# Kernel optimization log

Hardware: AMD Instinct MI355X
Metric: run time of the kernel (lower is better)

The kernel has to match this reference:

```python
import jax, jax.numpy as jnp
import numpy as np

FORGET_BIAS = 1.0

def _lstm_scan(x_seq, W, b, c0, h0):
    """x_seq: [T, B, D]; W: [D+H, 4H] (gate order i,j,f,o as in BasicLSTMCell)."""
    def step(carry, x_t):
        c, h = carry
        gates = jnp.dot(jnp.concatenate([x_t, h], axis=-1), W) + b  # [B, 4H]
        i, j, f, o = jnp.split(gates, 4, axis=-1)
        c_new = c * jax.nn.sigmoid(f + FORGET_BIAS) + jax.nn.sigmoid(i) * jnp.tanh(j)
        h_new = jnp.tanh(c_new) * jax.nn.sigmoid(o)
        return (c_new, h_new), h_new
    (c_T, h_T), hs = jax.lax.scan(step, (c0, h0), x_seq)
    return hs, (c_T, h_T)


def setup_inputs() -> dict:
    key = jax.random.key(0)
    ks = jax.random.split(key, 10)
    B, T_enc, D_in = 128, 64, 2048
    T_dec, D_w, H, V = 32, 300, 512, 32000
    s = lambda fan_in: 1.0 / np.sqrt(fan_in)
    return {
        "frames": jax.random.normal(ks[0], (B, T_enc, D_in), dtype=jnp.float32),
        "caption_ids": jax.random.randint(ks[1], (B, T_dec), 0, V, dtype=jnp.int32),
        "emb_table": jax.random.normal(ks[2], (V, D_w), dtype=jnp.float32) * 0.1,
        "W_enc": jax.random.normal(ks[3], (D_in + H, 4 * H), dtype=jnp.float32) * s(D_in + H),
        "b_enc": jnp.zeros((4 * H,), dtype=jnp.float32),
        "W_dec": jax.random.normal(ks[4], (D_w + H, 4 * H), dtype=jnp.float32) * s(D_w + H),
        "b_dec": jnp.zeros((4 * H,), dtype=jnp.float32),
        "W_out": jax.random.normal(ks[5], (H, D_w), dtype=jnp.float32) * s(H),
        "b_out": jnp.zeros((D_w,), dtype=jnp.float32),
    }


def reference(frames, caption_ids, emb_table, W_enc, b_enc, W_dec, b_dec, W_out, b_out):
    B, _, _ = frames.shape
    H = W_out.shape[0]
    c0 = jnp.zeros((B, H), dtype=frames.dtype)
    h0 = jnp.zeros((B, H), dtype=frames.dtype)

    # Encoder: dynamic_rnn over frames (dropout keep_prob=1 -> identity)
    _, enc_state = _lstm_scan(jnp.swapaxes(frames, 0, 1), W_enc, b_enc, c0, h0)

    # Decoder: teacher-forced over caption embeddings, starting from encoder state
    cap_emb = emb_table[caption_ids]                       # [B, T_dec, D_w]
    dec_hs, _ = _lstm_scan(jnp.swapaxes(cap_emb, 0, 1), W_dec, b_dec, *enc_state)  # [T_dec, B, H]

    # hidden_to_word dense per timestep
    word_vecs = jnp.einsum('tbh,hw->tbw', dec_hs, W_out) + b_out  # [T_dec, B, D_w]
    return jnp.swapaxes(word_vecs, 0, 1)                   # [B, T_dec, D_w]
```

## Files before the change

kernel.cpp:

```cpp
#include <hip/hip_runtime.h>
#include <stdint.h>

typedef unsigned short u16;
typedef __attribute__((ext_vector_type(4))) float f32x4;
typedef __attribute__((ext_vector_type(8))) short short8;
typedef __attribute__((ext_vector_type(4))) unsigned short u16x4;
typedef __attribute__((ext_vector_type(4))) int int4v;

__device__ __forceinline__ u16 f2b(float f) {
  uint32_t u = __float_as_uint(f);
  uint32_t r = (u + 0x7fffu + ((u >> 16) & 1u)) >> 16;
  return (u16)r;
}
__device__ __forceinline__ float b2f(u16 b) {
  return __uint_as_float(((uint32_t)b) << 16);
}
__device__ __forceinline__ float sigm(float x) { return 1.f / (1.f + __expf(-x)); }
__device__ __forceinline__ float tanh_fast(float x) {
  float e = __expf(2.f * x);
  return 1.f - 2.f / (e + 1.f);
}
__device__ __forceinline__ void gl2lds16(const void* g, void* l) {
  __builtin_amdgcn_global_load_lds((const __attribute__((address_space(1))) void*)g,
                                   (__attribute__((address_space(3))) void*)l, 16, 0, 0);
}

__global__ __launch_bounds__(256)
void prep_kernel(const float* __restrict__ frames, u16* __restrict__ A_enc,
                 const float* __restrict__ W_enc, u16* __restrict__ WencT,
                 const float* __restrict__ W_dec, u16* __restrict__ WdecT,
                 const float* __restrict__ W_out, u16* __restrict__ WoutT,
                 const int* __restrict__ ids, const float* __restrict__ emb,
                 u16* __restrict__ Adec) {
  __shared__ float tile[64][65];
  const int bid = blockIdx.x;
  const int tid = threadIdx.x;

  if (bid < 16384) {
    int i = bid * 256 + tid;
    float4 v = ((const float4*)frames)[i];
    int e = i * 4;
    int b = e >> 17;
    int t = (e >> 11) & 63;
    int d = e & 2047;
    size_t row = (size_t)t * 128 + b;
    u16x4 o = { f2b(v.x), f2b(v.y), f2b(v.z), f2b(v.w) };
    *(u16x4*)(A_enc + row * 2048 + d) = o;
    return;
  }

  const float* W; u16* WT; int ldin, ldout, xreal, xpad, bx, by;
  if (bid < 18080) {
    if (bid < 17664) {
      int idx = bid - 16384;
      W = W_enc; WT = WencT; ldin = 2048; ldout = 2560; xreal = 2048; xpad = 2048;
      bx = idx % 40; by = idx / 40;
    } else {
      int idx = bid - 17664;
      W = W_dec; WT = WdecT; ldin = 2048; ldout = 832; xreal = 300; xpad = 320;
      bx = idx % 13; by = idx / 13;
    }
    const int kb = bx * 64;
    const int pb = by * 64;
    const int pc = tid & 63;
    const int kr4 = tid >> 6;
#pragma unroll
    for (int it = 0; it < 16; ++it) {
      int kl = kr4 + it * 4;
      int kc = kb + kl;
      int ko = kc < xpad ? kc : kc - (xpad - xreal);
      bool valid = (kc < xreal) || (kc >= xpad);
      tile[kl][pc] = valid ? W[(size_t)ko * ldin + pb + pc] : 0.f;
    }
    __syncthreads();
    const int pl = tid >> 2;
    const int kq = tid & 3;
#pragma unroll
    for (int half = 0; half < 2; ++half) {
      union { short8 v; u16 a[8]; } pk;
#pragma unroll
      for (int i = 0; i < 8; ++i) pk.a[i] = f2b(tile[kq * 16 + half * 8 + i][pl]);
      *(short8*)&WT[(size_t)(pb + pl) * ldout + kb + kq * 16 + half * 8] = pk.v;
    }
    return;
  }

  if (bid < 18848) {
    int idx = (bid - 18080) * 256 + tid;
    int n = idx >> 9, k = idx & 511;
    float v = (n < 300) ? W_out[(size_t)k * 300 + n] : 0.f;
    WoutT[idx] = f2b(v);
    return;
  }

  int r = (bid - 18848) * 4 + (tid >> 6);
  int t = r >> 7, b = r & 127;
  int id = ids[b * 32 + t];
  const float* src = emb + (size_t)id * 300;
  u16* dst = Adec + (size_t)r * 320;
  for (int d = tid & 63; d < 320; d += 64)
    dst[d] = f2b(d < 300 ? src[d] : 0.f);
}

struct SmemLstm { u16 wlds[128][520]; u16 stage[2][16][32]; };
struct SmemGemm { u16 at[4][128 * 32]; u16 bt[4][128 * 32]; };
union SmemU { SmemLstm l; SmemGemm g; };

__global__ __launch_bounds__(256)
void mega_kernel(const u16* __restrict__ A_enc, const u16* __restrict__ WencT,
                 u16* __restrict__ pre_enc, const float* __restrict__ b_enc,
                 const u16* __restrict__ A_dec, const u16* __restrict__ WdecT,
                 u16* __restrict__ pre_dec, const float* __restrict__ b_dec,
                 const u16* __restrict__ WoutT, const float* __restrict__ b_out,
                 float* __restrict__ outp,
                 int* __restrict__ hbuf, u16* __restrict__ dec_hs,
                 int* __restrict__ flags, int* __restrict__ pf_enc,
                 int* __restrict__ pf_dec) {
  __shared__ SmemU sm;
  const int bid = blockIdx.x;
  const int tid = threadIdx.x;
  const int lane = tid & 63;

  if (bid < 128) {
    const int hb = tid >> 6;
    const int bg = bid & 7;
    const int hg = bid >> 3;
    const int colq = lane & 15;
    const int rquad = lane >> 4;

    for (int i = tid; i < 128 * 64; i += 256) {
      int lr = i >> 6, cc = i & 63;
      const u16* src = WencT + (size_t)((lr >> 5) * 512 + hg * 32 + (lr & 31)) * 2560 + 2048;
      *(short8*)&sm.l.wlds[lr][cc * 8] = *(const short8*)(src + cc * 8);
    }
    __syncthreads();

    float cst[4] = {0.f, 0.f, 0.f, 0.f};
    const int brow = bg * 16 + rquad * 4;
    const int pbase = hg * 32 + (hb & 1) * 16 + colq;
    union HV { int4v i; short8 s; };
    int pf_next = 0;

    for (int s = 0; s < 96; ++s) {
      const bool dec = (s >= 64);
      const int sb = s & 1;
      if (hb < 2) {
        const u16* pre_t = dec ? (pre_dec + (size_t)(s - 64) * 262144)
                               : (pre_enc + (size_t)s * 262144);
        if (pf_next != 16) {
          int* pf = dec ? (pf_dec + (s - 64)) : (pf_enc + s);
          while (__hip_atomic_load(pf, __ATOMIC_RELAXED, __HIP_MEMORY_SCOPE_AGENT) != 16) {}
        }
        asm volatile("" ::: "memory");
        int praw[4][4];
        const u16* p0 = pre_t + (size_t)brow * 2048 + pbase;
#pragma unroll
        for (int l = 0; l < 4; ++l)
#pragma unroll
          for (int r = 0; r < 4; ++r)
            asm volatile("global_load_ushort %0, %1, off sc0 sc1"
                         : "=v"(praw[l][r]) : "v"(p0 + (size_t)r * 2048 + l * 512) : "memory");
        if (s > 0) {
          const int* fp = flags + ((size_t)s * 8 + bg) * 16 + (lane & 15);
          while (__hip_atomic_load(fp, __ATOMIC_RELAXED, __HIP_MEMORY_SCOPE_AGENT) == 0) {}
          asm volatile("" ::: "memory");
        }
        HV hv[16];
        const int* hread = hbuf + (size_t)s * 32768 + bg * 4096 + colq * 16 + rquad * 4;
#pragma unroll
        for (int g = 0; g < 4; ++g) {
          const int* hp = hread + g * 1024;
#pragma unroll
          for (int q = 0; q < 4; ++q)
            asm volatile("global_load_dwordx4 %0, %1, off offset:%2 sc0 sc1"
                         : "=v"(hv[g * 4 + q].i) : "v"(hp), "i"(q * 1024) : "memory");
        }
        if (s + 1 < 96) {
          const int* pfn = (s + 1 >= 64) ? (pf_dec + (s + 1 - 64)) : (pf_enc + (s + 1));
          pf_next = __hip_atomic_load(pfn, __ATOMIC_RELAXED, __HIP_MEMORY_SCOPE_AGENT);
        }
        asm volatile("s_waitcnt vmcnt(0)" ::: "memory");
        __builtin_amdgcn_sched_barrier(0);
#pragma unroll
        for (int kt = 0; kt < 16; ++kt) asm volatile("" : "+v"(hv[kt].i));
#pragma unroll
        for (int l = 0; l < 4; ++l)
#pragma unroll
          for (int r = 0; r < 4; ++r) asm volatile("" : "+v"(praw[l][r]));
        f32x4 acc[4];
#pragma unroll
        for (int l = 0; l < 4; ++l)
#pragma unroll
          for (int r = 0; r < 4; ++r) acc[l][r] = b2f((u16)praw[l][r]);
#pragma unroll
        for (int kt = 0; kt < 16; ++kt) {
#pragma unroll
          for (int l = 0; l < 4; ++l) {
            short8 bf = *(const short8*)&sm.l.wlds[l * 32 + hb * 16 + colq][kt * 32 + rquad * 8];
            acc[l] = __builtin_amdgcn_mfma_f32_16x16x32_bf16(hv[kt].s, bf, acc[l], 0, 0, 0);
          }
        }
#pragma unroll
        for (int r = 0; r < 4; ++r) {
          float iv = acc[0][r], jv = acc[1][r], fv = acc[2][r], ov = acc[3][r];
          float cn = cst[r] * sigm(fv + 1.f) + sigm(iv) * tanh_fast(jv);
          cst[r] = cn;
          float hvv = tanh_fast(cn) * sigm(ov);
          sm.l.stage[sb][rquad * 4 + r][hb * 16 + colq] = f2b(hvv);
        }
      }
      __syncthreads();
      if (hb == 2) {
        const int t2 = tid - 128;
        const int row = t2 >> 2, q = t2 & 3;
        union { short8 v; int4v i; } vv;
        vv.v = *(const short8*)&sm.l.stage[sb][row][q * 8];
        int* dst = hbuf + (size_t)(s + 1) * 32768 + bg * 4096 + hg * 256 + row * 16 + q * 4;
        asm volatile("global_store_dwordx4 %0, %1, off sc0 sc1"
                     :: "v"(dst), "v"(vv.i) : "memory");
        if (dec) {
          const u16* da = dec_hs + (size_t)(s - 64) * 65536 +
                          (size_t)(bg * 16 + row) * 512 + hg * 32 + q * 8;
          asm volatile("global_store_dwordx4 %0, %1, off sc0 sc1"
                       :: "v"(da), "v"(vv.i) : "memory");
        }
        asm volatile("s_waitcnt vmcnt(0)" ::: "memory");
        if (t2 == 0) {
          int* fp = flags + ((size_t)(s + 1) * 8 + bg) * 16 + hg;
          int one = 1;
          asm volatile("global_store_dword %0, %1, off sc0 sc1"
                       :: "v"(fp), "v"(one) : "memory");
        }
      }
      if (s == 63) {
        for (int i = tid; i < 128 * 64; i += 256) {
          int lr = i >> 6, cc = i & 63;
          const u16* src = WdecT + (size_t)((lr >> 5) * 512 + hg * 32 + (lr & 31)) * 832 + 320;
          *(short8*)&sm.l.wlds[lr][cc * 8] = *(const short8*)(src + cc * 8);
        }
        __syncthreads();
      }
    }
    asm volatile("s_waitcnt vmcnt(0)" ::: "memory");
    return;
  }

  int idx = bid - 128;
  const u16* A; const u16* BT; u16* Cb = nullptr; const float* bias; int* flag = nullptr;
  int lda, ldb, K, m0, n0, mode, tcap = 0;
  if (idx < 1024) {
    int t = idx >> 4, nt = idx & 15;
    A = A_enc; lda = 2048; BT = WencT; ldb = 2560; K = 2048;
    Cb = pre_enc; bias = b_enc; flag = pf_enc + t;
    m0 = t * 128; n0 = nt * 128; mode = 0;
  } else if (idx < 1536) {
    idx -= 1024;
    int t = idx >> 4, nt = idx & 15;
    A = A_dec; lda = 320; BT = WdecT; ldb = 832; K = 320;
    Cb = pre_dec; bias = b_dec; flag = pf_dec + t;
    m0 = t * 128; n0 = nt * 128; mode = 0;
  } else {
    idx -= 1536;
    int t = idx / 3, nt = idx % 3;
    A = dec_hs; lda = 512; BT = WoutT; ldb = 512; K = 512;
    bias = b_out; m0 = t * 128; n0 = nt * 128; mode = 1; tcap = t;
    const int* wf = flags + (size_t)(tcap + 65) * 128 + (tid & 127);
    while (__hip_atomic_load(wf, __ATOMIC_RELAXED, __HIP_MEMORY_SCOPE_AGENT) == 0) {}
    asm volatile("" ::: "memory");
    __syncthreads();
  }
  const int wave = tid >> 6;
  const int wm = wave & 1, wn = wave >> 1;
  const int colq = lane & 15, rquad = lane >> 4;

  f32x4 acc[4][4];
#pragma unroll
  for (int i = 0; i < 4; ++i)
#pragma unroll
    for (int j = 0; j < 4; ++j) { f32x4 z = {0.f, 0.f, 0.f, 0.f}; acc[i][j] = z; }

  auto stage_tile = [&](int buf, int k0) {
#pragma unroll
    for (int c = 0; c < 2; ++c) {
      const int ch = wave + c * 4;
      const int slot = ch * 64 + lane;
      const int m = slot >> 2;
      const int koff = (slot & 3) * 8;
      gl2lds16(A + (size_t)(m0 + m) * lda + k0 + koff, sm.g.at[buf] + ch * 512);
      gl2lds16(BT + (size_t)(n0 + m) * ldb + k0 + koff, sm.g.bt[buf] + ch * 512);
    }
  };

  const int niter = K >> 5;
  stage_tile(0, 0);
  stage_tile(1, 32);
  stage_tile(2, 64);
  for (int it = 0; it < niter; ++it) {
    if (it + 3 < niter) stage_tile((it + 3) & 3, (it + 3) << 5);
    const int excess = (niter - 1 - it) < 3 ? (niter - 1 - it) : 3;
    if (excess == 3)      asm volatile("s_waitcnt vmcnt(12)" ::: "memory");
    else if (excess == 2) asm volatile("s_waitcnt vmcnt(8)" ::: "memory");
    else if (excess == 1) asm volatile("s_waitcnt vmcnt(4)" ::: "memory");
    else                  asm volatile("s_waitcnt vmcnt(0)" ::: "memory");
    __builtin_amdgcn_s_barrier();
    __builtin_amdgcn_sched_barrier(0);
    const int cur = it & 3;
    short8 af[4], bf[4];
#pragma unroll
    for (int i = 0; i < 4; ++i)
      af[i] = *(const short8*)(sm.g.at[cur] + (wm * 64 + i * 16 + colq) * 32 + rquad * 8);
#pragma unroll
    for (int j = 0; j < 4; ++j)
      bf[j] = *(const short8*)(sm.g.bt[cur] + (wn * 64 + j * 16 + colq) * 32 + rquad * 8);
#pragma unroll
    for (int i = 0; i < 4; ++i)
#pragma unroll
      for (int j = 0; j < 4; ++j)
        acc[i][j] = __builtin_amdgcn_mfma_f32_16x16x32_bf16(af[i], bf[j], acc[i][j], 0, 0, 0);
    __builtin_amdgcn_sched_barrier(0);
    asm volatile("s_waitcnt lgkmcnt(0)" ::: "memory");
    __builtin_amdgcn_s_barrier();
  }

  const int gm_base = m0 + wm * 64;
  const int gn_base = n0 + wn * 64;
  if (mode == 0) {
#pragma unroll
    for (int i = 0; i < 4; ++i) {
#pragma unroll
      for (int j = 0; j < 4; ++j) {
        const int gn = gn_base + j * 16 + colq;
        const float bv = bias[gn];
        const int rbase = gm_base + i * 16 + rquad * 4;
#pragma unroll
        for (int r = 0; r < 4; ++r) {
          int hv16 = (int)f2b(acc[i][j][r] + bv);
          const u16* addr = Cb + (size_t)(rbase + r) * 2048 + gn;
          asm volatile("global_store_short %0, %1, off sc0 sc1"
                       :: "v"(addr), "v"(hv16) : "memory");
        }
      }
    }
    asm volatile("s_waitcnt vmcnt(0)" ::: "memory");
    __syncthreads();
    if (tid == 0)
      __hip_atomic_fetch_add(flag, 1, __ATOMIC_RELAXED, __HIP_MEMORY_SCOPE_AGENT);
  } else {
#pragma unroll
    for (int i = 0; i < 4; ++i) {
#pragma unroll
      for (int j = 0; j < 4; ++j) {
        const int gn = gn_base + j * 16 + colq;
        const float bv = (gn < 300) ? bias[gn] : 0.f;
        const int rbase = gm_base + i * 16 + rquad * 4;
#pragma unroll
        for (int r = 0; r < 4; ++r) {
          const float v = acc[i][j][r] + bv;
          const int row = rbase + r;
          if (gn < 300)
            outp[(size_t)((row & 127) * 32 + (row >> 7)) * 300 + gn] = v;
        }
      }
    }
  }
}

extern "C" void kernel_launch(void* const* d_in, const int* in_sizes, int n_in,
                              void* d_out, int out_size, void* d_ws, size_t ws_size,
                              hipStream_t stream) {
  const float* frames = (const float*)d_in[0];
  const int* cap_ids  = (const int*)d_in[1];
  const float* emb    = (const float*)d_in[2];
  const float* W_enc  = (const float*)d_in[3];
  const float* b_enc  = (const float*)d_in[4];
  const float* W_dec  = (const float*)d_in[5];
  const float* b_dec  = (const float*)d_in[6];
  const float* W_out  = (const float*)d_in[7];
  const float* b_out  = (const float*)d_in[8];
  float* out = (float*)d_out;

  char* ws = (char*)d_ws;
  size_t off = 0;
  auto alloc = [&](size_t bytes) {
    void* p = ws + off;
    off += (bytes + 255) & ~(size_t)255;
    return p;
  };
  u16* A_enc   = (u16*)alloc(8192ull * 2048 * 2);
  u16* WencT   = (u16*)alloc(2048ull * 2560 * 2);
  u16* pre_enc = (u16*)alloc(64ull * 128 * 2048 * 2);
  u16* A_dec   = (u16*)alloc(4096ull * 320 * 2);
  u16* WdecT   = (u16*)alloc(2048ull * 832 * 2);
  u16* pre_dec = (u16*)alloc(32ull * 128 * 2048 * 2);
  u16* WoutT   = (u16*)alloc(384ull * 512 * 2);
  u16* dec_hs  = (u16*)alloc(32ull * 128 * 512 * 2);
  int* hbuf    = (int*)alloc(97ull * 32768 * 4);
  int* flags   = (int*)alloc(97ull * 8 * 16 * 4);
  int* pf      = (int*)alloc(96ull * 4);
  int* pf_enc  = pf;
  int* pf_dec  = pf + 64;

  hipMemsetAsync(hbuf, 0, 32768ull * 4, stream);
  hipMemsetAsync(flags, 0, 97ull * 8 * 16 * 4, stream);
  hipMemsetAsync(pf, 0, 96ull * 4, stream);

  prep_kernel<<<19872, 256, 0, stream>>>(frames, A_enc, W_enc, WencT, W_dec, WdecT,
                                         W_out, WoutT, cap_ids, emb, A_dec);

  mega_kernel<<<1760, 256, 0, stream>>>(A_enc, WencT, pre_enc, b_enc,
                                        A_dec, WdecT, pre_dec, b_dec,
                                        WoutT, b_out, out,
                                        hbuf, dec_hs, flags, pf_enc, pf_dec);
}
```

Measured before the change: 667.3 us.

## Store gate pre-activations in LSTM-consumer-friendly layout and add decoder-output flags

```diff
diff --git a/kernel.cpp b/kernel.cpp
--- a/kernel.cpp
+++ b/kernel.cpp
@@ -6,6 +6,7 @@
 typedef __attribute__((ext_vector_type(8))) short short8;
 typedef __attribute__((ext_vector_type(4))) unsigned short u16x4;
 typedef __attribute__((ext_vector_type(4))) int int4v;
+typedef __attribute__((ext_vector_type(2))) int int2v;
 
 __device__ __forceinline__ u16 f2b(float f) {
   uint32_t u = __float_as_uint(f);
@@ -115,7 +116,7 @@
                  float* __restrict__ outp,
                  int* __restrict__ hbuf, u16* __restrict__ dec_hs,
                  int* __restrict__ flags, int* __restrict__ pf_enc,
-                 int* __restrict__ pf_dec) {
+                 int* __restrict__ pf_dec, int* __restrict__ dflags) {
   __shared__ SmemU sm;
   const int bid = blockIdx.x;
   const int tid = threadIdx.x;
@@ -137,8 +138,9 @@
 
     float cst[4] = {0.f, 0.f, 0.f, 0.f};
     const int brow = bg * 16 + rquad * 4;
-    const int pbase = hg * 32 + (hb & 1) * 16 + colq;
+    const size_t pchunk = ((((size_t)(bg * 16 + hg) * 2 + (hb & 1)) * 4 + rquad) * 16 + colq) * 16;
     union HV { int4v i; short8 s; };
+    union PR { int4v i; u16 a[8]; };
     int pf_next = 0;
 
     for (int s = 0; s < 96; ++s) {
@@ -149,17 +151,16 @@
                                : (pre_enc + (size_t)s * 262144);
         if (pf_next != 16) {
           int* pf = dec ? (pf_dec + (s - 64)) : (pf_enc + s);
-          while (__hip_atomic_load(pf, __ATOMIC_RELAXED, __HIP_MEMORY_SCOPE_AGENT) != 16) {}
+          while (__hip_atomic_load(pf, __ATOMIC_RELAXED, __HIP_MEMORY_SCOPE_AGENT) != 16)
+            __builtin_amdgcn_s_sleep(1);
         }
         asm volatile("" ::: "memory");
-        int praw[4][4];
-        const u16* p0 = pre_t + (size_t)brow * 2048 + pbase;
-#pragma unroll
-        for (int l = 0; l < 4; ++l)
-#pragma unroll
-          for (int r = 0; r < 4; ++r)
-            asm volatile("global_load_ushort %0, %1, off sc0 sc1"
-                         : "=v"(praw[l][r]) : "v"(p0 + (size_t)r * 2048 + l * 512) : "memory");
+        PR praw[2];
+        const u16* p0 = pre_t + pchunk;
+        asm volatile("global_load_dwordx4 %0, %1, off sc0 sc1"
+                     : "=v"(praw[0].i) : "v"(p0) : "memory");
+        asm volatile("global_load_dwordx4 %0, %1, off offset:16 sc0 sc1"
+                     : "=v"(praw[1].i) : "v"(p0) : "memory");
         if (s > 0) {
           const int* fp = flags + ((size_t)s * 8 + bg) * 16 + (lane & 15);
           while (__hip_atomic_load(fp, __ATOMIC_RELAXED, __HIP_MEMORY_SCOPE_AGENT) == 0) {}
@@ -183,15 +184,15 @@
         __builtin_amdgcn_sched_barrier(0);
 #pragma unroll
         for (int kt = 0; kt < 16; ++kt) asm volatile("" : "+v"(hv[kt].i));
+        asm volatile("" : "+v"(praw[0].i), "+v"(praw[1].i));
+        f32x4 acc[4];
 #pragma unroll
         for (int l = 0; l < 4; ++l)
 #pragma unroll
-          for (int r = 0; r < 4; ++r) asm volatile("" : "+v"(praw[l][r]));
-        f32x4 acc[4];
-#pragma unroll
-        for (int l = 0; l < 4; ++l)
-#pragma unroll
-          for (int r = 0; r < 4; ++r) acc[l][r] = b2f((u16)praw[l][r]);
+          for (int r = 0; r < 4; ++r) {
+            int e = l * 4 + r;
+            acc[l][r] = b2f(praw[e >> 3].a[e & 7]);
+          }
 #pragma unroll
         for (int kt = 0; kt < 16; ++kt) {
 #pragma unroll
@@ -231,6 +232,12 @@
           asm volatile("global_store_dword %0, %1, off sc0 sc1"
                        :: "v"(fp), "v"(one) : "memory");
         }
+        if (dec && t2 == 1) {
+          int* dfp = dflags + (size_t)(s - 64) * 128 + bid;
+          int one = 1;
+          asm volatile("global_store_dword %0, %1, off sc0 sc1"
+                       :: "v"(dfp), "v"(one) : "memory");
+        }
       }
       if (s == 63) {
         for (int i = tid; i < 128 * 64; i += 256) {
@@ -247,25 +254,28 @@
 
   int idx = bid - 128;
   const u16* A; const u16* BT; u16* Cb = nullptr; const float* bias; int* flag = nullptr;
-  int lda, ldb, K, m0, n0, mode, tcap = 0;
+  int lda, ldb, K, m0, n0, mode;
   if (idx < 1024) {
     int t = idx >> 4, nt = idx & 15;
     A = A_enc; lda = 2048; BT = WencT; ldb = 2560; K = 2048;
-    Cb = pre_enc; bias = b_enc; flag = pf_enc + t;
+    Cb = pre_enc + (size_t)t * 262144; bias = b_enc; flag = pf_enc + t;
     m0 = t * 128; n0 = nt * 128; mode = 0;
   } else if (idx < 1536) {
     idx -= 1024;
     int t = idx >> 4, nt = idx & 15;
     A = A_dec; lda = 320; BT = WdecT; ldb = 832; K = 320;
-    Cb = pre_dec; bias = b_dec; flag = pf_dec + t;
+    Cb = pre_dec + (size_t)t * 262144; bias = b_dec; flag = pf_dec + t;
     m0 = t * 128; n0 = nt * 128; mode = 0;
   } else {
     idx -= 1536;
     int t = idx / 3, nt = idx % 3;
     A = dec_hs; lda = 512; BT = WoutT; ldb = 512; K = 512;
-    bias = b_out; m0 = t * 128; n0 = nt * 128; mode = 1; tcap = t;
-    const int* wf = flags + (size_t)(tcap + 65) * 128 + (tid & 127);
-    while (__hip_atomic_load(wf, __ATOMIC_RELAXED, __HIP_MEMORY_SCOPE_AGENT) == 0) {}
+    bias = b_out; m0 = t * 128; n0 = nt * 128; mode = 1;
+    if (tid < 128) {
+      const int* wf = dflags + (size_t)t * 128 + tid;
+      while (__hip_atomic_load(wf, __ATOMIC_RELAXED, __HIP_MEMORY_SCOPE_AGENT) == 0)
+        __builtin_amdgcn_s_sleep(8);
+    }
     asm volatile("" ::: "memory");
     __syncthreads();
   }
@@ -327,18 +337,23 @@
   if (mode == 0) {
 #pragma unroll
     for (int i = 0; i < 4; ++i) {
+      const int bgp = wm * 4 + i;
 #pragma unroll
       for (int j = 0; j < 4; ++j) {
-        const int gn = gn_base + j * 16 + colq;
+        const int gnb = gn_base + j * 16;
+        const int gn = gnb + colq;
         const float bv = bias[gn];
-        const int rbase = gm_base + i * 16 + rquad * 4;
-#pragma unroll
-        for (int r = 0; r < 4; ++r) {
-          int hv16 = (int)f2b(acc[i][j][r] + bv);
-          const u16* addr = Cb + (size_t)(rbase + r) * 2048 + gn;
-          asm volatile("global_store_short %0, %1, off sc0 sc1"
-                       :: "v"(addr), "v"(hv16) : "memory");
-        }
+        const int l = gnb >> 9;
+        const int hcolb = gnb & 511;
+        const int hg_ = hcolb >> 5;
+        const int hb_ = (hcolb >> 4) & 1;
+        u16* cp = Cb + ((((size_t)(bgp * 16 + hg_) * 2 + hb_) * 4 + rquad) * 16 + colq) * 16
+                     + l * 4;
+        union { u16x4 h; int2v d; } pk;
+#pragma unroll
+        for (int r = 0; r < 4; ++r) pk.h[r] = f2b(acc[i][j][r] + bv);
+        asm volatile("global_store_dwordx2 %0, %1, off sc0 sc1"
+                     :: "v"(cp), "v"(pk.d) : "memory");
       }
     }
     asm volatile("s_waitcnt vmcnt(0)" ::: "memory");
@@ -397,12 +412,14 @@
   int* hbuf    = (int*)alloc(97ull * 32768 * 4);
   int* flags   = (int*)alloc(97ull * 8 * 16 * 4);
   int* pf      = (int*)alloc(96ull * 4);
+  int* dflags  = (int*)alloc(32ull * 128 * 4);
   int* pf_enc  = pf;
   int* pf_dec  = pf + 64;
 
   hipMemsetAsync(hbuf, 0, 32768ull * 4, stream);
   hipMemsetAsync(flags, 0, 97ull * 8 * 16 * 4, stream);
   hipMemsetAsync(pf, 0, 96ull * 4, stream);
+  hipMemsetAsync(dflags, 0, 32ull * 128 * 4, stream);
 
   prep_kernel<<<19872, 256, 0, stream>>>(frames, A_enc, W_enc, WencT, W_dec, WdecT,
                                          W_out, WoutT, cap_ids, emb, A_dec);
@@ -410,5 +427,5 @@
   mega_kernel<<<1760, 256, 0, stream>>>(A_enc, WencT, pre_enc, b_enc,
                                         A_dec, WdecT, pre_dec, b_dec,
                                         WoutT, b_out, out,
-                                        hbuf, dec_hs, flags, pf_enc, pf_dec);
-}
+                                        hbuf, dec_hs, flags, pf_enc, pf_dec, dflags);
+}
```

Result: no change. 664.9 us (-0.4%).
